# Optimization experiments

Hardware: AMD Instinct MI355X
Metric: run time of the kernel (lower is better)

## Reference

```python
import jax, jax.numpy as jnp
import numpy as np

N = 100_000      # nodes
E = 400_000      # edges
NPERM = 100_000  # local receptive-field subgraphs
L = 16           # lrp_length
H = 64           # hid_dim
NLAYERS = 4
G = 1024         # graphs in the batch
P = NPERM * L    # permutation rows (must be NPERM * L)


def _spmm(row, col, val, mat, m):
    # COO sparse [m, n] @ dense [n, d]  (torch_sparse.spmm equivalent)
    return jax.ops.segment_sum(val[:, None] * mat[col], row, num_segments=m)


def setup_inputs() -> dict:
    key = jax.random.key(0)
    ks = jax.random.split(key, 16)
    inp = {}
    inp["node_feat"] = jax.random.normal(ks[0], (N, 28), jnp.float32)
    inp["degs"] = jax.random.uniform(ks[1], (N,), jnp.float32) * 8.0
    inp["batch"] = jnp.sort(jax.random.randint(ks[2], (N,), 0, G)).astype(jnp.int32)
    # node -> perm-length permutation matrix (one nonzero per perm row)
    inp["n2p_row"] = jnp.arange(P, dtype=jnp.int32)
    inp["n2p_col"] = jax.random.randint(ks[3], (P,), 0, N, dtype=jnp.int32)
    inp["n2p_val"] = jnp.ones((P,), jnp.float32)
    # edge -> perm-length permutation matrix
    inp["e2p_row"] = jnp.arange(P, dtype=jnp.int32)
    inp["e2p_col"] = jax.random.randint(ks[4], (P,), 0, E, dtype=jnp.int32)
    inp["e2p_val"] = jnp.ones((P,), jnp.float32)
    # pooling matrix: subgraph row -> root node, shape [N, NPERM]
    inp["pool_row"] = jax.random.randint(ks[5], (NPERM,), 0, N, dtype=jnp.int32)
    inp["pool_col"] = jnp.arange(NPERM, dtype=jnp.int32)
    inp["pool_val"] = jax.random.uniform(ks[6], (NPERM,), jnp.float32)
    # parameters
    inp["atom_W"] = jax.random.normal(ks[7], (28, H), jnp.float32) * 0.1
    inp["atom_b"] = jnp.zeros((H,), jnp.float32)
    inp["edge_W"] = jax.random.normal(ks[8], (1, H), jnp.float32) * 0.1
    inp["edge_b"] = jnp.zeros((H,), jnp.float32)
    inp["W_lrp"] = jax.random.normal(ks[9], (NLAYERS, H, H, L), jnp.float32) * 0.03
    inp["b_lrp"] = jnp.zeros((NLAYERS, H), jnp.float32)
    inp["dn0_W"] = jax.random.normal(ks[10], (NLAYERS, 1, 2 * H), jnp.float32) * 0.2
    inp["dn0_b"] = jnp.zeros((NLAYERS, 2 * H), jnp.float32)
    inp["dn1_W"] = jax.random.normal(ks[11], (NLAYERS, 2 * H, H), jnp.float32) * 0.1
    inp["dn1_b"] = jnp.zeros((NLAYERS, H), jnp.float32)
    return inp


def reference(node_feat, degs, batch,
              n2p_row, n2p_col, n2p_val,
              e2p_row, e2p_col, e2p_val,
              pool_row, pool_col, pool_val,
              atom_W, atom_b, edge_W, edge_b,
              W_lrp, b_lrp, dn0_W, dn0_b, dn1_W, dn1_b):
    x = node_feat @ atom_W + atom_b                       # atom_encoder  [N, H]
    # all edge features are 1 -> edge_encoder gives identical rows
    efeat = jnp.ones((E, 1), node_feat.dtype) @ edge_W + edge_b  # [E, H]
    for i in range(NLAYERS):
        # gather nodes + edges into perm-length layout   [P, H]
        perm = _spmm(n2p_row, n2p_col, n2p_val, x, P) \
             + _spmm(e2p_row, e2p_col, e2p_val, efeat, P)
        # transpose(0,1).view(H,-1,L).permute(1,2,0) == reshape(NPERM, L, H)
        t = perm.reshape(NPERM, L, H)
        # einsum('dab,bca->dc') with weights [H_in, H_out, L]
        h = jax.nn.relu(jnp.einsum('plh,hcl->pc', t, W_lrp[i]) + b_lrp[i])  # [NPERM, H]
        pooled = _spmm(pool_row, pool_col, pool_val, h, N)  # [N, H]
        hid = jax.nn.relu(degs[:, None] @ dn0_W[i] + dn0_b[i])  # [N, 2H]
        factor = hid @ dn1_W[i] + dn1_b[i]                      # [N, H]
        x = pooled * factor
    # global mean pool over graphs
    sums = jax.ops.segment_sum(x, batch, num_segments=G)
    cnts = jax.ops.segment_sum(jnp.ones((x.shape[0],), x.dtype), batch, num_segments=G)
    return sums / jnp.maximum(cnts, 1.0)[:, None]
```

## Files before the change

### kernel.cpp

```cpp
#include <hip/hip_runtime.h>

typedef __attribute__((ext_vector_type(8))) short bf16x8;
typedef __attribute__((ext_vector_type(4))) float f32x4;

#define N_NODES   100000
#define NPERM_    100000
#define L_        16
#define G_        1024
#define CAP_      20
#define OVF_MAX   4096

__device__ inline unsigned short f32_to_bf16(float f) {
    unsigned u = __float_as_uint(f);
    unsigned r = (u + 0x7fff + ((u >> 16) & 1)) >> 16;
    return (unsigned short)r;
}
__device__ inline float bflo(unsigned u) { return __uint_as_float(u << 16); }
__device__ inline float bfhi(unsigned u) { return __uint_as_float(u & 0xffff0000u); }
__device__ inline float bfup(unsigned short s) { return __uint_as_float((unsigned)s << 16); }
__device__ inline unsigned pk2(float a, float b) {
    return (unsigned)f32_to_bf16(a) | ((unsigned)f32_to_bf16(b) << 16);
}

__global__ __launch_bounds__(256) void k_prep_w(const float* __restrict__ W,
                                                unsigned short* __restrict__ Wh,
                                                unsigned short* __restrict__ Wl) {
    int o = blockIdx.x * 256 + threadIdx.x;
    int k = o & 63, c = (o >> 6) & 63, l = (o >> 12) & 15, i = o >> 16;
    float f = W[(((i * 64 + k) * 64) + c) * 16 + l];
    unsigned short hh = f32_to_bf16(f);
    float fl = f - __uint_as_float(((unsigned)hh) << 16);
    Wh[o] = hh;
    Wl[o] = f32_to_bf16(fl);
}

__global__ __launch_bounds__(256) void k_prep_factor(const float* __restrict__ dn0_W,
                                                     const float* __restrict__ dn0_b,
                                                     const float* __restrict__ dn1_W,
                                                     const float* __restrict__ dn1_b,
                                                     float* __restrict__ tab,
                                                     float* __restrict__ thr) {
    int i     = blockIdx.x;
    int chunk = blockIdx.y;
    int tid   = threadIdx.x;
    __shared__ float A[128], B[128], ts[128], tv[128];
    __shared__ float W1l[128 * 64];
    if (tid < 128) { A[tid] = dn0_W[i * 128 + tid]; B[tid] = dn0_b[i * 128 + tid]; }
    {
        const float4* src = (const float4*)(dn1_W + (size_t)i * 8192);
        float4*       dst = (float4*)W1l;
        for (int t = tid; t < 2048; t += 256) dst[t] = src[t];
    }
    __syncthreads();
    if (tid < 128) {
        float a = A[tid], b = B[tid];
        float tj = -b / a;
        if (a == 0.f || !(tj > 0.f)) tj = 1e30f;
        tv[tid] = tj;
    }
    __syncthreads();
    if (tid < 128) {
        float tj = tv[tid];
        int rank = 0;
        for (int j = 0; j < 128; ++j) {
            float o = tv[j];
            rank += (o < tj) || (o == tj && j < tid);
        }
        ts[rank] = tj;
    }
    __syncthreads();
    if (chunk == 0 && tid < 128) thr[i * 128 + tid] = ts[tid];
    int s0 = chunk * 17;
    int s1 = min(s0 + 17, 129);
    float* tb = tab + (size_t)i * 129 * 128;
    for (int item = s0 * 64 + tid; item < s1 * 64; item += 256) {
        int s = item >> 6;
        int c = item & 63;
        float lo = (s == 0) ? 0.f : ts[s - 1];
        float hi = (s == 128) ? 1e30f : ts[s];
        float g;
        if (lo > 1e29f)       g = 1e29f;
        else if (hi > 1e29f)  g = lo + 1.f;
        else                  g = 0.5f * (lo + hi);
        float alpha = 0.f, beta = dn1_b[i * 64 + c];
        for (int j = 0; j < 128; ++j) {
            if (fmaf(g, A[j], B[j]) > 0.f) {
                float w1 = W1l[j * 64 + c];
                alpha = fmaf(A[j], w1, alpha);
                beta  = fmaf(B[j], w1, beta);
            }
        }
        tb[s * 128 + c * 2 + 0] = alpha;
        tb[s * 128 + c * 2 + 1] = beta;
    }
}

__global__ __launch_bounds__(256) void k_atom(const float* __restrict__ feat,
                                              const float* __restrict__ W,
                                              const float* __restrict__ b,
                                              unsigned short* __restrict__ xb) {
    __shared__ float Wlds[28 * 64];
    __shared__ float blds[64];
    int tid = threadIdx.x;
    for (int t = tid; t < 28 * 64; t += 256) Wlds[t] = W[t];
    if (tid < 64) blds[tid] = b[tid];
    __syncthreads();
    int n = blockIdx.x * 4 + (tid >> 6);
    int c = tid & 63;
    if (n >= N_NODES) return;
    const float* fr = feat + n * 28;
    float acc = blds[c];
#pragma unroll
    for (int j = 0; j < 28; ++j) acc = fmaf(fr[j], Wlds[j * 64 + c], acc);
    xb[n * 64 + c] = f32_to_bf16(acc);
}

__global__ __launch_bounds__(256) void k_bucket(const int* __restrict__ prow,
                                                int* __restrict__ cntn,
                                                int* __restrict__ bucket,
                                                int* __restrict__ ovf,
                                                int* __restrict__ ovfc) {
    int d = blockIdx.x * 256 + threadIdx.x;
    if (d >= NPERM_) return;
    int n = prow[d];
    int s = atomicAdd(cntn + n, 1);
    if (s < CAP_) bucket[n * CAP_ + s] = d;
    else { int o = atomicAdd(ovfc, 1); if (o < OVF_MAX) ovf[o] = d; }
}

__global__ __launch_bounds__(256, 5) void k_lrp(const unsigned short* __restrict__ xbuf,
                                                const int*   __restrict__ n2p_col,
                                                const float* __restrict__ n2p_val,
                                                const float* __restrict__ e2p_val,
                                                const float* __restrict__ edge_W,
                                                const float* __restrict__ edge_b,
                                                const unsigned short* __restrict__ Wth,
                                                const unsigned short* __restrict__ Wtl,
                                                const float* __restrict__ bl,
                                                unsigned short* __restrict__ hout) {
    __shared__ unsigned short Tb[64][72];
    __shared__ unsigned short Wh[64][72];
    __shared__ unsigned short Wo[64][72];
    __shared__ float efs[64];
    int tid = threadIdx.x;
    int lane = tid & 63;
    int w = tid >> 6;
    int d0 = blockIdx.x * 64;
    int dl = tid >> 2;
    int kq = tid & 3;
    int wc = tid >> 2;
    int wk = (tid & 3) * 16;
    int dg = d0 + dl;
    int dsafe = (dg < NPERM_) ? dg : 0;
    size_t pbase = (size_t)dsafe * 16;

    if (tid < 64) efs[tid] = edge_W[tid] + edge_b[tid];

    f32x4 acc[4];
#pragma unroll
    for (int cb = 0; cb < 4; ++cb) acc[cb] = (f32x4)0.f;

    uint4 xvA[2], xvB[2], wvh0, wvh1, wvl0, wvl1;
    int   colN  = n2p_col[pbase + 2];
    int   colN2 = n2p_col[pbase + 3];
    float vnN   = n2p_val[pbase + 0];
    float veN   = e2p_val[pbase + 0];
    {
        int c0 = n2p_col[pbase + 0];
        int c1 = n2p_col[pbase + 1];
        const uint4* xr0 = (const uint4*)(xbuf + (size_t)c0 * 64 + kq * 16);
        xvA[0] = xr0[0]; xvA[1] = xr0[1];
        const uint4* xr1 = (const uint4*)(xbuf + (size_t)c1 * 64 + kq * 16);
        xvB[0] = xr1[0]; xvB[1] = xr1[1];
        const uint4* whr = (const uint4*)(Wth + wc * 64 + wk);
        wvh0 = whr[0]; wvh1 = whr[1];
        const uint4* wlr = (const uint4*)(Wtl + wc * 64 + wk);
        wvl0 = wlr[0]; wvl1 = wlr[1];
    }
    __syncthreads();

#define LRP_PHASE(LVAL, XV)                                                      \
    {                                                                            \
        const int l = (LVAL);                                                    \
        float vn = vnN, ve = veN;                                                \
        __syncthreads();                                                         \
        _Pragma("unroll")                                                        \
        for (int j = 0; j < 2; ++j) {                                            \
            uint4 v = XV[j];                                                     \
            int kb = kq * 16 + j * 8;                                            \
            float4 ea = *(const float4*)&efs[kb];                                \
            float4 eb = *(const float4*)&efs[kb + 4];                            \
            float t0 = fmaf(vn, bflo(v.x), ve * ea.x);                           \
            float t1 = fmaf(vn, bfhi(v.x), ve * ea.y);                           \
            float t2 = fmaf(vn, bflo(v.y), ve * ea.z);                           \
            float t3 = fmaf(vn, bfhi(v.y), ve * ea.w);                           \
            float t4 = fmaf(vn, bflo(v.z), ve * eb.x);                           \
            float t5 = fmaf(vn, bfhi(v.z), ve * eb.y);                           \
            float t6 = fmaf(vn, bflo(v.w), ve * eb.z);                           \
            float t7 = fmaf(vn, bfhi(v.w), ve * eb.w);                           \
            uint4 ow;                                                            \
            ow.x = pk2(t0, t1); ow.y = pk2(t2, t3);                              \
            ow.z = pk2(t4, t5); ow.w = pk2(t6, t7);                              \
            *(uint4*)&Tb[dl][kb] = ow;                                           \
        }                                                                        \
        *(uint4*)&Wh[wc][wk]     = wvh0;                                         \
        *(uint4*)&Wh[wc][wk + 8] = wvh1;                                         \
        *(uint4*)&Wo[wc][wk]     = wvl0;                                         \
        *(uint4*)&Wo[wc][wk + 8] = wvl1;                                         \
        __syncthreads();                                                         \
        if (l < 15) {                                                            \
            const uint4* whr = (const uint4*)(Wth + (l + 1) * 4096 + wc * 64 + wk); \
            wvh0 = whr[0]; wvh1 = whr[1];                                        \
            const uint4* wlr = (const uint4*)(Wtl + (l + 1) * 4096 + wc * 64 + wk); \
            wvl0 = wlr[0]; wvl1 = wlr[1];                                        \
            vnN = n2p_val[pbase + l + 1];                                        \
            veN = e2p_val[pbase + l + 1];                                        \
        }                                                                        \
        if (l < 14) {           \
            const uint4* xr = (const uint4*)(xbuf + (size_t)colN * 64 + kq * 16);\
            XV[0] = xr[0]; XV[1] = xr[1];                                        \
            colN = colN2;                                                        \
            if (l < 12) colN2 = n2p_col[pbase + l + 4];                          \
        }                                                                        \
        {                                                                        \
            int r = lane & 15, q = lane >> 4;                                    \
            _Pragma("unroll")                                                    \
            for (int s = 0; s < 2; ++s) {                                        \
                int ko = s * 32 + q * 8;                                         \
                bf16x8 a0 = *(const bf16x8*)&Tb[w * 16 + r][ko];                 \
                _Pragma("unroll")                                                \
                for (int cb = 0; cb < 4; ++cb) {                                 \
                    bf16x8 bh = *(const bf16x8*)&Wh[cb * 16 + r][ko];            \
                    bf16x8 bo = *(const bf16x8*)&Wo[cb * 16 + r][ko];            \
                    acc[cb] = __builtin_amdgcn_mfma_f32_16x16x32_bf16(a0, bh, acc[cb], 0, 0, 0); \
                    acc[cb] = __builtin_amdgcn_mfma_f32_16x16x32_bf16(a0, bo, acc[cb], 0, 0, 0); \
                }                                                                \
            }                                                                    \
        }                                                                        \
    }

#pragma unroll 1
    for (int lp = 0; lp < 8; ++lp) {
        LRP_PHASE(2 * lp,     xvA)
        LRP_PHASE(2 * lp + 1, xvB)
    }
#undef LRP_PHASE

    __syncthreads();
    {
        int r = lane & 15, q = lane >> 4;
        unsigned short* F = &Tb[0][0] + w * 1024;
#pragma unroll
        for (int cb = 0; cb < 4; ++cb) {
            float bias = bl[cb * 16 + r];
#pragma unroll
            for (int reg = 0; reg < 4; ++reg)
                F[(q * 4 + reg) * 64 + cb * 16 + r] =
                    f32_to_bf16(fmaxf(acc[cb][reg] + bias, 0.f));
        }
#pragma unroll
        for (int ii = 0; ii < 2; ++ii) {
            int idx = lane + ii * 64;
            uint4 v = ((const uint4*)F)[idx];
            int R = d0 + w * 16 + (idx >> 3);
            if (R < NPERM_)
                *(uint4*)(hout + (size_t)R * 64 + (idx & 7) * 8) = v;
        }
    }
}

__global__ __launch_bounds__(256) void k_pool_seg(const unsigned short* __restrict__ h,
                                                  const int*   __restrict__ cntn,
                                                  const int*   __restrict__ bucket,
                                                  const int*   __restrict__ ovf,
                                                  const int*   __restrict__ ovfc,
                                                  const int*   __restrict__ prow,
                                                  const float* __restrict__ pval,
                                                  const float* __restrict__ degs,
                                                  const float* __restrict__ tab,
                                                  const float* __restrict__ thr,
                                                  float* __restrict__ x,
                                                  unsigned short* __restrict__ xbo,
                                                  int last) {
    __shared__ float thrl[128];
    int tid = threadIdx.x;
    if (tid < 128) thrl[tid] = thr[tid];
    __syncthreads();
    int n  = blockIdx.x * 16 + (tid >> 4);
    int c4 = (tid & 15) * 4;
    if (n >= N_NODES) return;
    float dgv = degs[n];
    int seg = 0;
    if (thrl[63]       < dgv) seg = 64;
    if (thrl[seg + 31] < dgv) seg += 32;
    if (thrl[seg + 15] < dgv) seg += 16;
    if (thrl[seg + 7]  < dgv) seg += 8;
    if (thrl[seg + 3]  < dgv) seg += 4;
    if (thrl[seg + 1]  < dgv) seg += 2;
    if (thrl[seg]      < dgv) seg += 1;
    float4 p = make_float4(0.f, 0.f, 0.f, 0.f);
    int cn = min(cntn[n], CAP_);
    for (int j = 0; j < cn; ++j) {
        int   d  = bucket[n * CAP_ + j];
        float pv = pval[d];
        ushort4 hv = *(const ushort4*)(h + (size_t)d * 64 + c4);
        p.x = fmaf(pv, bfup(hv.x), p.x);
        p.y = fmaf(pv, bfup(hv.y), p.y);
        p.z = fmaf(pv, bfup(hv.z), p.z);
        p.w = fmaf(pv, bfup(hv.w), p.w);
    }
    int novf = *ovfc;
    if (novf > 0) {
        int ne = novf < OVF_MAX ? novf : OVF_MAX;
        for (int e = 0; e < ne; ++e) {
            int d = ovf[e];
            if (prow[d] == n) {
                float pv = pval[d];
                ushort4 hv = *(const ushort4*)(h + (size_t)d * 64 + c4);
                p.x = fmaf(pv, bfup(hv.x), p.x);
                p.y = fmaf(pv, bfup(hv.y), p.y);
                p.z = fmaf(pv, bfup(hv.z), p.z);
                p.w = fmaf(pv, bfup(hv.w), p.w);
            }
        }
    }
    const float4* tf = (const float4*)(tab + (size_t)(seg * 64 + c4) * 2);
    float4 t0 = tf[0], t1 = tf[1];
    float4 xo;
    xo.x = p.x * fmaf(t0.x, dgv, t0.y);
    xo.y = p.y * fmaf(t0.z, dgv, t0.w);
    xo.z = p.z * fmaf(t1.x, dgv, t1.y);
    xo.w = p.w * fmaf(t1.z, dgv, t1.w);
    if (last) {
        *(float4*)(x + (size_t)n * 64 + c4) = xo;
    } else {
        ushort4 s;
        s.x = f32_to_bf16(xo.x); s.y = f32_to_bf16(xo.y);
        s.z = f32_to_bf16(xo.z); s.w = f32_to_bf16(xo.w);
        *(ushort4*)(xbo + (size_t)n * 64 + c4) = s;
    }
}

__global__ __launch_bounds__(256) void k_gpool(const float* __restrict__ x,
                                               const int* __restrict__ batch,
                                               float* __restrict__ out,
                                               float* __restrict__ cnt) {
    int wave = (blockIdx.x * 256 + threadIdx.x) >> 6;
    int lane = threadIdx.x & 63;
    int n0 = wave * 64;
    if (n0 >= N_NODES) return;
    int n1 = min(n0 + 64, N_NODES);
    int g = batch[n0];
    float s = 0.f, c = 0.f;
    for (int n = n0; n < n1; ++n) {
        int gn = batch[n];
        if (gn != g) {
            atomicAdd(out + (size_t)g * 64 + lane, s);
            if (lane == 0) atomicAdd(cnt + g, c);
            s = 0.f; c = 0.f; g = gn;
        }
        s += x[(size_t)n * 64 + lane];
        c += 1.f;
    }
    atomicAdd(out + (size_t)g * 64 + lane, s);
    if (lane == 0) atomicAdd(cnt + g, c);
}

__global__ __launch_bounds__(256) void k_gdiv(float* __restrict__ out,
                                              const float* __restrict__ cnt) {
    int idx = blockIdx.x * 256 + threadIdx.x;
    if (idx >= G_ * 64) return;
    out[idx] /= fmaxf(cnt[idx >> 6], 1.f);
}

extern "C" void kernel_launch(void* const* d_in, const int* in_sizes, int n_in,
                              void* d_out, int out_size, void* d_ws, size_t ws_size,
                              hipStream_t stream) {
    const float* node_feat = (const float*)d_in[0];
    const float* degs      = (const float*)d_in[1];
    const int*   batch     = (const int*)  d_in[2];
    const int*   n2p_col   = (const int*)  d_in[4];
    const float* n2p_val   = (const float*)d_in[5];
    const float* e2p_val   = (const float*)d_in[8];
    const int*   pool_row  = (const int*)  d_in[9];
    const float* pool_val  = (const float*)d_in[11];
    const float* atom_W    = (const float*)d_in[12];
    const float* atom_b    = (const float*)d_in[13];
    const float* edge_W    = (const float*)d_in[14];
    const float* edge_b    = (const float*)d_in[15];
    const float* W_lrp     = (const float*)d_in[16];
    const float* b_lrp     = (const float*)d_in[17];
    const float* dn0_W     = (const float*)d_in[18];
    const float* dn0_b     = (const float*)d_in[19];
    const float* dn1_W     = (const float*)d_in[20];
    const float* dn1_b     = (const float*)d_in[21];

    char* ws = (char*)d_ws;
    unsigned short* h      = (unsigned short*)(ws);
    unsigned short* xb     = (unsigned short*)(ws + 12800000);
    unsigned short* Wth    = (unsigned short*)(ws + 25600000);
    unsigned short* Wtl    = (unsigned short*)(ws + 26124288);
    int*            bucket = (int*)           (ws + 26648576);
    int*            cntn   = (int*)           (ws + 34648576);
    int*            ovf    = (int*)           (ws + 35048576);
    int*            ovfc   = (int*)           (ws + 35064960);
    float*          tab    = (float*)         (ws + 35065088);
    float*          thr    = (float*)         (ws + 35329280);
    float*          cntg   = (float*)         (ws + 35331328);
    float*          x      = (float*)         (ws + 35335424);

    hipLaunchKernelGGL(k_prep_w, dim3(1024), dim3(256), 0, stream, W_lrp, Wth, Wtl);
    hipLaunchKernelGGL(k_prep_factor, dim3(4, 8), dim3(256), 0, stream,
                       dn0_W, dn0_b, dn1_W, dn1_b, tab, thr);
    hipLaunchKernelGGL(k_atom, dim3(25000), dim3(256), 0, stream,
                       node_feat, atom_W, atom_b, xb);
    hipMemsetAsync(cntn, 0, 416512, stream);
    hipLaunchKernelGGL(k_bucket, dim3(391), dim3(256), 0, stream,
                       pool_row, cntn, bucket, ovf, ovfc);
    for (int i = 0; i < 4; ++i) {
        hipLaunchKernelGGL(k_lrp, dim3(1563), dim3(256), 0, stream,
                           xb, n2p_col, n2p_val, e2p_val, edge_W, edge_b,
                           Wth + (size_t)i * 65536, Wtl + (size_t)i * 65536,
                           b_lrp + i * 64, h);
        hipLaunchKernelGGL(k_pool_seg, dim3(6250), dim3(256), 0, stream,
                           h, cntn, bucket, ovf, ovfc, pool_row, pool_val,
                           degs, tab + (size_t)i * 129 * 128, thr + i * 128,
                           x, xb, (i == 3) ? 1 : 0);
    }
    hipMemsetAsync(d_out, 0, (size_t)G_ * 64 * 4, stream);
    hipMemsetAsync(cntg, 0, G_ * 4, stream);
    hipLaunchKernelGGL(k_gpool, dim3(391), dim3(256), 0, stream,
                       x, batch, (float*)d_out, cntg);
    hipLaunchKernelGGL(k_gdiv, dim3(256), dim3(256), 0, stream,
                       (float*)d_out, cntg);
}
```

Before: 596.6 us.

## Stage LRP operands via direct global-to-LDS loads with double-buffered MFMA-fragment layout

Weights are pre-permuted into a fragment-ordered interleaved hi/lo buffer so each lane reads its MFMA B operand contiguously. The x gathers and weight tiles now go straight from global memory into LDS through global_load_lds, double-buffered one step ahead. Each wave builds its own A fragment in registers instead of writing a shared transposed tile. This removes the register staging and one barrier per step, at the cost of more LDS, lower declared occupancy (launch bounds 5 to 3), and relying on global_load_lds lane-to-LDS placement semantics.

Result: slower. 675.9 us (+13.3%).

```diff
diff --git a/kernel.cpp b/kernel.cpp
--- a/kernel.cpp
+++ b/kernel.cpp
@@ -22,16 +22,27 @@
     return (unsigned)f32_to_bf16(a) | ((unsigned)f32_to_bf16(b) << 16);
 }
 
+typedef __attribute__((address_space(1))) const unsigned int gas_u32;
+typedef __attribute__((address_space(3))) unsigned int las_u32;
+__device__ __forceinline__ void gld16(const void* g, void* l) {
+    __builtin_amdgcn_global_load_lds((gas_u32*)g, (las_u32*)l, 16, 0, 0);
+}
+
 __global__ __launch_bounds__(256) void k_prep_w(const float* __restrict__ W,
-                                                unsigned short* __restrict__ Wh,
-                                                unsigned short* __restrict__ Wl) {
+                                                unsigned short* __restrict__ Wt2) {
     int o = blockIdx.x * 256 + threadIdx.x;
-    int k = o & 63, c = (o >> 6) & 63, l = (o >> 12) & 15, i = o >> 16;
+    int j    = o & 7;
+    int lane = (o >> 3) & 63;
+    int sc   = (o >> 9) & 7;
+    int l    = (o >> 12) & 15;
+    int ho   = (o >> 16) & 1;
+    int i    = o >> 17;
+    int s = sc >> 2, cb = sc & 3;
+    int k = s * 32 + (lane >> 4) * 8 + j;
+    int c = cb * 16 + (lane & 15);
     float f = W[(((i * 64 + k) * 64) + c) * 16 + l];
     unsigned short hh = f32_to_bf16(f);
-    float fl = f - __uint_as_float(((unsigned)hh) << 16);
-    Wh[o] = hh;
-    Wl[o] = f32_to_bf16(fl);
+    Wt2[o] = ho ? f32_to_bf16(f - bfup(hh)) : hh;
 }
 
 __global__ __launch_bounds__(256) void k_prep_factor(const float* __restrict__ dn0_W,
@@ -128,128 +139,96 @@
     else { int o = atomicAdd(ovfc, 1); if (o < OVF_MAX) ovf[o] = d; }
 }
 
-__global__ __launch_bounds__(256, 5) void k_lrp(const unsigned short* __restrict__ xbuf,
+__global__ __launch_bounds__(256, 3) void k_lrp(const unsigned short* __restrict__ xbuf,
                                                 const int*   __restrict__ n2p_col,
                                                 const float* __restrict__ n2p_val,
                                                 const float* __restrict__ e2p_val,
                                                 const float* __restrict__ edge_W,
                                                 const float* __restrict__ edge_b,
-                                                const unsigned short* __restrict__ Wth,
-                                                const unsigned short* __restrict__ Wtl,
+                                                const unsigned short* __restrict__ Wt2,
                                                 const float* __restrict__ bl,
                                                 unsigned short* __restrict__ hout) {
-    __shared__ unsigned short Tb[64][72];
-    __shared__ unsigned short Wh[64][72];
-    __shared__ unsigned short Wo[64][72];
-    __shared__ float efs[64];
+    __shared__ unsigned short Tb[2][4][2][512];
+    __shared__ unsigned short Wb[2][2][8][512];
     int tid = threadIdx.x;
     int lane = tid & 63;
     int w = tid >> 6;
+    int r = lane & 15, q = lane >> 4;
     int d0 = blockIdx.x * 64;
-    int dl = tid >> 2;
-    int kq = tid & 3;
-    int wc = tid >> 2;
-    int wk = (tid & 3) * 16;
-    int dg = d0 + dl;
-    int dsafe = (dg < NPERM_) ? dg : 0;
-    size_t pbase = (size_t)dsafe * 16;
-
-    if (tid < 64) efs[tid] = edge_W[tid] + edge_b[tid];
+    int myrow = w * 16 + r;
+    int dg = min(d0 + myrow, NPERM_ - 1);
+    size_t pbase = (size_t)dg * 16;
+
+    float efr[2][8];
+#pragma unroll
+    for (int s = 0; s < 2; ++s) {
+        int kb = s * 32 + q * 8;
+        float4 wa = *(const float4*)(edge_W + kb);
+        float4 wc = *(const float4*)(edge_W + kb + 4);
+        float4 ba = *(const float4*)(edge_b + kb);
+        float4 bc = *(const float4*)(edge_b + kb + 4);
+        efr[s][0] = wa.x + ba.x; efr[s][1] = wa.y + ba.y;
+        efr[s][2] = wa.z + ba.z; efr[s][3] = wa.w + ba.w;
+        efr[s][4] = wc.x + bc.x; efr[s][5] = wc.y + bc.y;
+        efr[s][6] = wc.z + bc.z; efr[s][7] = wc.w + bc.w;
+    }
 
     f32x4 acc[4];
 #pragma unroll
     for (int cb = 0; cb < 4; ++cb) acc[cb] = (f32x4)0.f;
 
-    uint4 xvA[2], xvB[2], wvh0, wvh1, wvl0, wvl1;
-    int   colN  = n2p_col[pbase + 2];
-    int   colN2 = n2p_col[pbase + 3];
-    float vnN   = n2p_val[pbase + 0];
-    float veN   = e2p_val[pbase + 0];
+    auto stage = [&](int l, int buf, int col) {
+        const unsigned short* ap = xbuf + (size_t)col * 64 + q * 8;
+        gld16(ap,      &Tb[buf][w][0][0]);
+        gld16(ap + 32, &Tb[buf][w][1][0]);
+        const unsigned short* wl = Wt2 + l * 4096;
+#pragma unroll
+        for (int i = 0; i < 4; ++i) {
+            int c = w * 4 + i;
+            gld16(wl + (c >> 3) * 65536 + (c & 7) * 512 + lane * 8,
+                  &Wb[buf][c >> 3][c & 7][0]);
+        }
+    };
+
+    int colA = n2p_col[pbase + 0];
+    stage(0, 0, colA);
+    colA = n2p_col[pbase + 1];
+    float vnC = n2p_val[pbase + 0], veC = e2p_val[pbase + 0];
+    __syncthreads();
+
+#pragma unroll 1
+    for (int l = 0; l < L_; ++l) {
+        int buf = l & 1;
+        if (l < 15) stage(l + 1, buf ^ 1, colA);
+        if (l < 14) colA = n2p_col[pbase + l + 2];
+        float vn = vnC, ve = veC;
+        if (l < 15) { vnC = n2p_val[pbase + l + 1]; veC = e2p_val[pbase + l + 1]; }
+#pragma unroll
+        for (int s = 0; s < 2; ++s) {
+            uint4 v = *(const uint4*)&Tb[buf][w][s][lane * 8];
+            uint4 aw;
+            aw.x = pk2(fmaf(vn, bflo(v.x), ve * efr[s][0]),
+                       fmaf(vn, bfhi(v.x), ve * efr[s][1]));
+            aw.y = pk2(fmaf(vn, bflo(v.y), ve * efr[s][2]),
+                       fmaf(vn, bfhi(v.y), ve * efr[s][3]));
+            aw.z = pk2(fmaf(vn, bflo(v.z), ve * efr[s][4]),
+                       fmaf(vn, bfhi(v.z), ve * efr[s][5]));
+            aw.w = pk2(fmaf(vn, bflo(v.w), ve * efr[s][6]),
+                       fmaf(vn, bfhi(v.w), ve * efr[s][7]));
+            bf16x8 a0 = *(bf16x8*)&aw;
+#pragma unroll
+            for (int cb = 0; cb < 4; ++cb) {
+                bf16x8 bh = *(const bf16x8*)&Wb[buf][0][s * 4 + cb][lane * 8];
+                bf16x8 bo = *(const bf16x8*)&Wb[buf][1][s * 4 + cb][lane * 8];
+                acc[cb] = __builtin_amdgcn_mfma_f32_16x16x32_bf16(a0, bh, acc[cb], 0, 0, 0);
+                acc[cb] = __builtin_amdgcn_mfma_f32_16x16x32_bf16(a0, bo, acc[cb], 0, 0, 0);
+            }
+        }
+        __syncthreads();
+    }
+
     {
-        int c0 = n2p_col[pbase + 0];
-        int c1 = n2p_col[pbase + 1];
-        const uint4* xr0 = (const uint4*)(xbuf + (size_t)c0 * 64 + kq * 16);
-        xvA[0] = xr0[0]; xvA[1] = xr0[1];
-        const uint4* xr1 = (const uint4*)(xbuf + (size_t)c1 * 64 + kq * 16);
-        xvB[0] = xr1[0]; xvB[1] = xr1[1];
-        const uint4* whr = (const uint4*)(Wth + wc * 64 + wk);
-        wvh0 = whr[0]; wvh1 = whr[1];
-        const uint4* wlr = (const uint4*)(Wtl + wc * 64 + wk);
-        wvl0 = wlr[0]; wvl1 = wlr[1];
-    }
-    __syncthreads();
-
-#define LRP_PHASE(LVAL, XV)                                                      \
-    {                                                                            \
-        const int l = (LVAL);                                                    \
-        float vn = vnN, ve = veN;                                                \
-        __syncthreads();                                                         \
-        _Pragma("unroll")                                                        \
-        for (int j = 0; j < 2; ++j) {                                            \
-            uint4 v = XV[j];                                                     \
-            int kb = kq * 16 + j * 8;                                            \
-            float4 ea = *(const float4*)&efs[kb];                                \
-            float4 eb = *(const float4*)&efs[kb + 4];                            \
-            float t0 = fmaf(vn, bflo(v.x), ve * ea.x);                           \
-            float t1 = fmaf(vn, bfhi(v.x), ve * ea.y);                           \
-            float t2 = fmaf(vn, bflo(v.y), ve * ea.z);                           \
-            float t3 = fmaf(vn, bfhi(v.y), ve * ea.w);                           \
-            float t4 = fmaf(vn, bflo(v.z), ve * eb.x);                           \
-            float t5 = fmaf(vn, bfhi(v.z), ve * eb.y);                           \
-            float t6 = fmaf(vn, bflo(v.w), ve * eb.z);                           \
-            float t7 = fmaf(vn, bfhi(v.w), ve * eb.w);                           \
-            uint4 ow;                                                            \
-            ow.x = pk2(t0, t1); ow.y = pk2(t2, t3);                              \
-            ow.z = pk2(t4, t5); ow.w = pk2(t6, t7);                              \
-            *(uint4*)&Tb[dl][kb] = ow;                                           \
-        }                                                                        \
-        *(uint4*)&Wh[wc][wk]     = wvh0;                                         \
-        *(uint4*)&Wh[wc][wk + 8] = wvh1;                                         \
-        *(uint4*)&Wo[wc][wk]     = wvl0;                                         \
-        *(uint4*)&Wo[wc][wk + 8] = wvl1;                                         \
-        __syncthreads();                                                         \
-        if (l < 15) {                                                            \
-            const uint4* whr = (const uint4*)(Wth + (l + 1) * 4096 + wc * 64 + wk); \
-            wvh0 = whr[0]; wvh1 = whr[1];                                        \
-            const uint4* wlr = (const uint4*)(Wtl + (l + 1) * 4096 + wc * 64 + wk); \
-            wvl0 = wlr[0]; wvl1 = wlr[1];                                        \
-            vnN = n2p_val[pbase + l + 1];                                        \
-            veN = e2p_val[pbase + l + 1];                                        \
-        }                                                                        \
-        if (l < 14) {           \
-            const uint4* xr = (const uint4*)(xbuf + (size_t)colN * 64 + kq * 16);\
-            XV[0] = xr[0]; XV[1] = xr[1];                                        \
-            colN = colN2;                                                        \
-            if (l < 12) colN2 = n2p_col[pbase + l + 4];                          \
-        }                                                                        \
-        {                                                                        \
-            int r = lane & 15, q = lane >> 4;                                    \
-            _Pragma("unroll")                                                    \
-            for (int s = 0; s < 2; ++s) {                                        \
-                int ko = s * 32 + q * 8;                                         \
-                bf16x8 a0 = *(const bf16x8*)&Tb[w * 16 + r][ko];                 \
-                _Pragma("unroll")                                                \
-                for (int cb = 0; cb < 4; ++cb) {                                 \
-                    bf16x8 bh = *(const bf16x8*)&Wh[cb * 16 + r][ko];            \
-                    bf16x8 bo = *(const bf16x8*)&Wo[cb * 16 + r][ko];            \
-                    acc[cb] = __builtin_amdgcn_mfma_f32_16x16x32_bf16(a0, bh, acc[cb], 0, 0, 0); \
-                    acc[cb] = __builtin_amdgcn_mfma_f32_16x16x32_bf16(a0, bo, acc[cb], 0, 0, 0); \
-                }                                                                \
-            }                                                                    \
-        }                                                                        \
-    }
-
-#pragma unroll 1
-    for (int lp = 0; lp < 8; ++lp) {
-        LRP_PHASE(2 * lp,     xvA)
-        LRP_PHASE(2 * lp + 1, xvB)
-    }
-#undef LRP_PHASE
-
-    __syncthreads();
-    {
-        int r = lane & 15, q = lane >> 4;
-        unsigned short* F = &Tb[0][0] + w * 1024;
+        unsigned short* F = &Tb[0][0][0][0] + w * 1024;
 #pragma unroll
         for (int cb = 0; cb < 4; ++cb) {
             float bias = bl[cb * 16 + r];
@@ -398,8 +377,7 @@
     char* ws = (char*)d_ws;
     unsigned short* h      = (unsigned short*)(ws);
     unsigned short* xb     = (unsigned short*)(ws + 12800000);
-    unsigned short* Wth    = (unsigned short*)(ws + 25600000);
-    unsigned short* Wtl    = (unsigned short*)(ws + 26124288);
+    unsigned short* Wt2    = (unsigned short*)(ws + 25600000);
     int*            bucket = (int*)           (ws + 26648576);
     int*            cntn   = (int*)           (ws + 34648576);
     int*            ovf    = (int*)           (ws + 35048576);
@@ -409,7 +387,7 @@
     float*          cntg   = (float*)         (ws + 35331328);
     float*          x      = (float*)         (ws + 35335424);
 
-    hipLaunchKernelGGL(k_prep_w, dim3(1024), dim3(256), 0, stream, W_lrp, Wth, Wtl);
+    hipLaunchKernelGGL(k_prep_w, dim3(2048), dim3(256), 0, stream, W_lrp, Wt2);
     hipLaunchKernelGGL(k_prep_factor, dim3(4, 8), dim3(256), 0, stream,
                        dn0_W, dn0_b, dn1_W, dn1_b, tab, thr);
     hipLaunchKernelGGL(k_atom, dim3(25000), dim3(256), 0, stream,
@@ -420,8 +398,7 @@
     for (int i = 0; i < 4; ++i) {
         hipLaunchKernelGGL(k_lrp, dim3(1563), dim3(256), 0, stream,
                            xb, n2p_col, n2p_val, e2p_val, edge_W, edge_b,
-                           Wth + (size_t)i * 65536, Wtl + (size_t)i * 65536,
-                           b_lrp + i * 64, h);
+                           Wt2 + (size_t)i * 131072, b_lrp + i * 64, h);
         hipLaunchKernelGGL(k_pool_seg, dim3(6250), dim3(256), 0, stream,
                            h, cntn, bucket, ovf, ovfc, pool_row, pool_val,
                            degs, tab + (size_t)i * 129 * 128, thr + i * 128,
```
